# Kernel optimization log

Hardware: AMD Instinct MI355X
Metric: run time of the kernel (lower is better)

The kernel has to match this reference:

```python
import jax, jax.numpy as jnp
import numpy as np

D_MODEL = 1024
NHEAD = 16
D_FF = 4096
SEQ = 2048
BATCH = 2
EPS = 1e-5


def _layernorm(x, g, b):
    mu = jnp.mean(x, axis=-1, keepdims=True)
    var = jnp.var(x, axis=-1, keepdims=True)
    return (x - mu) * jax.lax.rsqrt(var + EPS) * g + b


def setup_inputs() -> dict:
    key = jax.random.key(0)
    ks = jax.random.split(key, 16)
    s = 0.02
    def lin(k, din, dout):
        return jax.random.normal(k, (din, dout), jnp.float32) * s
    return {
        "x": jax.random.normal(ks[0], (SEQ, BATCH, D_MODEL), jnp.float32),
        "Wq": lin(ks[1], D_MODEL, D_MODEL), "bq": jnp.zeros((D_MODEL,), jnp.float32),
        "Wk": lin(ks[2], D_MODEL, D_MODEL), "bk": jnp.zeros((D_MODEL,), jnp.float32),
        "Wv": lin(ks[3], D_MODEL, D_MODEL), "bv": jnp.zeros((D_MODEL,), jnp.float32),
        "Wo": lin(ks[4], D_MODEL, D_MODEL), "bo": jnp.zeros((D_MODEL,), jnp.float32),
        "W1": lin(ks[5], D_MODEL, D_FF), "b1": jnp.zeros((D_FF,), jnp.float32),
        "W2": lin(ks[6], D_FF, D_MODEL), "b2": jnp.zeros((D_MODEL,), jnp.float32),
        "g1": jnp.ones((D_MODEL,), jnp.float32), "be1": jnp.zeros((D_MODEL,), jnp.float32),
        "g2": jnp.ones((D_MODEL,), jnp.float32), "be2": jnp.zeros((D_MODEL,), jnp.float32),
    }


def reference(x, Wq, bq, Wk, bk, Wv, bv, Wo, bo, W1, b1, W2, b2, g1, be1, g2, be2):
    # batch_first=False: x is [S, B, D] -> [B, S, D]
    xb = jnp.transpose(x, (1, 0, 2))
    B, S, D = xb.shape
    H, Dh = NHEAD, D // NHEAD

    Q = (xb @ Wq + bq).reshape(B, S, H, Dh)
    K = (xb @ Wk + bk).reshape(B, S, H, Dh)
    V = (xb @ Wv + bv).reshape(B, S, H, Dh)

    scores = jnp.einsum('bqhd,bkhd->bhqk', Q, K) / jnp.sqrt(jnp.float32(Dh))
    attn = jax.nn.softmax(scores, axis=-1)
    ctx = jnp.einsum('bhqk,bkhd->bqhd', attn, V).reshape(B, S, D)

    x_att = ctx @ Wo + bo
    xb = xb + x_att
    xb = _layernorm(xb, g1, be1)  # post-norm (norm_first=False)

    h = jax.nn.gelu(xb @ W1 + b1, approximate=False)
    xb = xb + (h @ W2 + b2)
    xb = _layernorm(xb, g2, be2)

    return jnp.transpose(xb, (1, 0, 2))  # back to [S, B, D]
```

## Files before the change

### kernel.cpp

```cpp
#include <hip/hip_runtime.h>
#include <hip/hip_bf16.h>
#include <cstdint>
#include <cstddef>

#define S_LEN 2048
#define BATCHN 2
#define DMODEL 1024
#define NHEADS 16
#define DHEAD 64
#define DFF 4096
#define NTOK (S_LEN*BATCHN)

typedef __bf16 bf16x8 __attribute__((ext_vector_type(8)));
typedef __bf16 bf16x4 __attribute__((ext_vector_type(4)));
typedef float f32x4 __attribute__((ext_vector_type(4)));
typedef __hip_bfloat16 bf16s;

#define QSCALE 0.18033688011112042592f

__device__ static inline void gload_lds16(const void* g, void* l) {
  __builtin_amdgcn_global_load_lds((const __attribute__((address_space(1))) void*)g,
                                   (__attribute__((address_space(3))) void*)l,
                                   16, 0, 0);
}


__global__ __launch_bounds__(256) void transpose_convert4(const float* __restrict__ s0,
                                                          const float* __restrict__ s1,
                                                          const float* __restrict__ s2,
                                                          const float* __restrict__ s3,
                                                          bf16s* __restrict__ dst) {
  __shared__ float tile[32][33];
  const float* in = (blockIdx.z == 0) ? s0 : (blockIdx.z == 1) ? s1 : (blockIdx.z == 2) ? s2 : s3;
  bf16s* out = dst + (size_t)blockIdx.z * DMODEL * DMODEL;
  const int tx = threadIdx.x & 31;
  const int ty = threadIdx.x >> 5;
  const int bx = blockIdx.x * 32;
  const int by = blockIdx.y * 32;
#pragma unroll
  for (int i = 0; i < 32; i += 8)
    tile[ty + i][tx] = in[(size_t)(by + ty + i) * DMODEL + bx + tx];
  __syncthreads();
#pragma unroll
  for (int i = 0; i < 32; i += 8)
    out[(size_t)(bx + ty + i) * DMODEL + by + tx] = __float2bfloat16(tile[tx][ty + i]);
}

__global__ __launch_bounds__(256) void transpose_convert(const float* __restrict__ in,
                                                         bf16s* __restrict__ out,
                                                         int K, int N) {
  __shared__ float tile[32][33];
  const int tx = threadIdx.x & 31;
  const int ty = threadIdx.x >> 5;
  const int bx = blockIdx.x * 32;
  const int by = blockIdx.y * 32;
#pragma unroll
  for (int i = 0; i < 32; i += 8)
    tile[ty + i][tx] = in[(size_t)(by + ty + i) * N + bx + tx];
  __syncthreads();
#pragma unroll
  for (int i = 0; i < 32; i += 8)
    out[(size_t)(bx + ty + i) * K + by + tx] = __float2bfloat16(tile[tx][ty + i]);
}

__global__ __launch_bounds__(256) void cvt_bf16_kernel(const float* __restrict__ in,
                                                       bf16s* __restrict__ out, int n4) {
  int i = blockIdx.x * 256 + threadIdx.x;
  if (i < n4) {
    float4 v = ((const float4*)in)[i];
    union { bf16s h[4]; uint2 u; } pk;
    pk.h[0] = __float2bfloat16(v.x); pk.h[1] = __float2bfloat16(v.y);
    pk.h[2] = __float2bfloat16(v.z); pk.h[3] = __float2bfloat16(v.w);
    ((uint2*)out)[i] = pk.u;
  }
}

__global__ __launch_bounds__(256) void bias_concat_kernel(const float* __restrict__ bq,
                                                          const float* __restrict__ bk,
                                                          const float* __restrict__ bv,
                                                          float* __restrict__ bqkv) {
  int i = blockIdx.x * 256 + threadIdx.x;
  if (i < 3 * DMODEL) {
    float v = (i < DMODEL) ? bq[i] : (i < 2 * DMODEL ? bk[i - DMODEL] : bv[i - 2 * DMODEL]);
    bqkv[i] = v;
  }
}

template<int EPI>
__global__ __launch_bounds__(256, 3)
void gemm_kernel(const bf16s* __restrict__ A, const bf16s* __restrict__ Bt,
                 int N, int K, int kchunk,
                 const float* __restrict__ bias,
                 float* __restrict__ outF, bf16s* __restrict__ outB,
                 bf16s* __restrict__ Qb, bf16s* __restrict__ Kb, bf16s* __restrict__ Vtb)
{
  __shared__ bf16s smem[2][8192];
  const int tid = threadIdx.x;
  const int l = tid & 63, w = tid >> 6;
  const int m0 = blockIdx.y * 128;
  const int n0 = blockIdx.x * 128;
  const int kbeg = blockIdx.z * kchunk;
  const int lr = l & 15, lg = l >> 4;
  const int wm = (w >> 1) * 64, wn = (w & 1) * 64;

  const int off0 = (w * 2 + 0) * 1024 + l * 16;
  const int off1 = (w * 2 + 1) * 1024 + l * 16;
  const char* a0 = (const char*)(A + (size_t)(m0 + (off0 >> 6)) * K + kbeg) + (off0 & 63);
  const char* a1 = (const char*)(A + (size_t)(m0 + (off1 >> 6)) * K + kbeg) + (off1 & 63);
  const char* b0 = (const char*)(Bt + (size_t)(n0 + (off0 >> 6)) * K + kbeg) + (off0 & 63);
  const char* b1 = (const char*)(Bt + (size_t)(n0 + (off1 >> 6)) * K + kbeg) + (off1 & 63);

  f32x4 acc[4][4] = {};

  auto stage = [&](int buf, int t) {
    char* s = (char*)&smem[buf][0];
    size_t kb = (size_t)t * 64;
    gload_lds16(a0 + kb, s + off0);
    gload_lds16(a1 + kb, s + off1);
    gload_lds16(b0 + kb, s + 8192 + off0);
    gload_lds16(b1 + kb, s + 8192 + off1);
  };

  const int ao = (wm + lr) * 64 + lg * 16;
  const int bo = 8192 + (wn + lr) * 64 + lg * 16;

  auto compute = [&](int buf) {
    const char* base = (const char*)&smem[buf][0];
    bf16x8 af[4], bfr[4];
#pragma unroll
    for (int mi = 0; mi < 4; ++mi) af[mi] = *(const bf16x8*)(base + ao + mi * 1024);
#pragma unroll
    for (int ni = 0; ni < 4; ++ni) bfr[ni] = *(const bf16x8*)(base + bo + ni * 1024);
#pragma unroll
    for (int mi = 0; mi < 4; ++mi)
#pragma unroll
      for (int ni = 0; ni < 4; ++ni)
        acc[mi][ni] = __builtin_amdgcn_mfma_f32_16x16x32_bf16(af[mi], bfr[ni], acc[mi][ni], 0, 0, 0);
  };

  const int nt = kchunk / 32;
  stage(0, 0);
  __syncthreads();
  int cur = 0;
  for (int t = 0; t < nt - 1; ++t) {
    stage(cur ^ 1, t + 1);
    compute(cur);
    __syncthreads();
    cur ^= 1;
  }
  compute(cur);

  float* outFz = (EPI == 1) ? outF + (size_t)blockIdx.z * ((size_t)NTOK * DMODEL) : outF;
#pragma unroll
  for (int mi = 0; mi < 4; ++mi) {
#pragma unroll
    for (int ni = 0; ni < 4; ++ni) {
#pragma unroll
      for (int r = 0; r < 4; ++r) {
        int row = m0 + wm + mi * 16 + lg * 4 + r;
        int col = n0 + wn + ni * 16 + lr;
        float v = acc[mi][ni][r];
        if (EPI == 0) {
          v += bias[col];
          int which = col >> 10;
          int h = (col & 1023) >> 6;
          int d = col & 63;
          int b = row & 1;
          int s = row >> 1;
          if (which == 0)
            Qb[(((size_t)(b * NHEADS + h)) * S_LEN + s) * DHEAD + d] = __float2bfloat16(v * QSCALE);
          else if (which == 1)
            Kb[(((size_t)(b * NHEADS + h)) * S_LEN + s) * DHEAD + d] = __float2bfloat16(v);
          else
            Vtb[(((size_t)(b * NHEADS + h)) * DHEAD + d) * S_LEN + s] = __float2bfloat16(v);
        } else if (EPI == 1) {
          outFz[(size_t)row * N + col] = v;
        } else {
          v += bias[col];
          float gv = 0.5f * v * (1.0f + erff(v * 0.70710678118654752f));
          outB[(size_t)row * N + col] = __float2bfloat16(gv);
        }
      }
    }
  }
}

__global__ __launch_bounds__(256, 2)
void attn_kernel(const bf16s* __restrict__ Qb, const bf16s* __restrict__ Kb,
                 const bf16s* __restrict__ Vtb, bf16s* __restrict__ ctx)
{
  __shared__ __align__(1024) char lds[51200];
  const int tid = threadIdx.x;
  const int l = tid & 63, w = tid >> 6;
  const int lr = l & 15, lg = l >> 4;

  int lin = blockIdx.x;
  int wg = (lin & 7) * 64 + (lin >> 3);
  int qb = wg & 15;
  int hb = wg >> 4;
  int h = hb & 15, b = hb >> 4;

  const char* Qg = (const char*)(Qb + ((size_t)(b * NHEADS + h)) * S_LEN * DHEAD);
  const char* Kg = (const char*)(Kb + ((size_t)(b * NHEADS + h)) * S_LEN * DHEAD);
  const char* Vg = (const char*)(Vtb + ((size_t)(b * NHEADS + h)) * DHEAD * S_LEN);

  const int swz = (lr & 7) << 4;
  const int aK0 = lr * 128 + ((lg * 16) ^ swz);
  const int aK1 = lr * 128 + ((64 + lg * 16) ^ swz);
  const int klane = (l >> 3) * 128  + (((l & 7) * 16) ^ ((l & 56) << 1));
  const int vlane = (l >> 3) * 4096 + (((l & 7) * 16) ^ ((l & 56) << 1));
  const int l16 = l * 16;
  char* Pw = lds + 32768 + w * 4608;
  const int pwA = lr * 144 + lg * 8;
  const int prA = lr * 144 + lg * 16;

  const int q0 = qb * 128 + w * 32;
  bf16x8 aq[2][2];
#pragma unroll
  for (int qi = 0; qi < 2; ++qi)
#pragma unroll
    for (int kk = 0; kk < 2; ++kk)
      aq[qi][kk] = *(const bf16x8*)(Qg + (size_t)(q0 + qi * 16 + lr) * 128 + kk * 64 + lg * 16);

  f32x4 o0[4] = {}, o1[4] = {};
  float m0 = -1e30f, m1 = -1e30f;
  float ls0 = 0.f, ls1 = 0.f;

  const int NT = S_LEN / 64;

  auto stage = [&](char* dK, int tile) {
    const char* kbg = Kg + (size_t)tile * 8192;
    const char* vbg = Vg + (size_t)tile * 128;
    char* dV = dK + 8192;
#pragma unroll
    for (int i = 0; i < 2; ++i) {
      int c = w * 2 + i;
      gload_lds16(kbg + c * 1024 + klane, dK + c * 1024 + l16);
      gload_lds16(vbg + (size_t)c * 32768 + vlane, dV + c * 1024 + l16);
    }
  };

  stage(lds, 0);
  asm volatile("s_waitcnt vmcnt(0)" ::: "memory");
  __builtin_amdgcn_s_barrier();

#define ATTN_ITER(BUF, t)                                                        \
  {                                                                              \
    int nxt = ((t) + 1 < NT) ? (t) + 1 : NT - 1;                                 \
    stage(lds + ((BUF) ^ 1) * 16384, nxt);                                       \
    const char* bK = lds + (BUF) * 16384;                                        \
    const char* bV = bK + 8192;                                                  \
    f32x4 st0[4], st1[4];                                                        \
    _Pragma("unroll")                                                            \
    for (int ni = 0; ni < 4; ++ni) {                                             \
      bf16x8 k0 = *(const bf16x8*)(bK + ni * 2048 + aK0);                        \
      bf16x8 k1 = *(const bf16x8*)(bK + ni * 2048 + aK1);                        \
      f32x4 z = {};                                                              \
      st0[ni] = __builtin_amdgcn_mfma_f32_16x16x32_bf16(k0, aq[0][0], z, 0, 0, 0);\
      st0[ni] = __builtin_amdgcn_mfma_f32_16x16x32_bf16(k1, aq[0][1], st0[ni], 0, 0, 0);\
      st1[ni] = __builtin_amdgcn_mfma_f32_16x16x32_bf16(k0, aq[1][0], z, 0, 0, 0);\
      st1[ni] = __builtin_amdgcn_mfma_f32_16x16x32_bf16(k1, aq[1][1], st1[ni], 0, 0, 0);\
    }                                                                            \
    f32x4 vm0 = st0[0], vm1 = st1[0];                                            \
    _Pragma("unroll")                                                            \
    for (int ni = 1; ni < 4; ++ni) {                                             \
      _Pragma("unroll")                                                          \
      for (int r = 0; r < 4; ++r) {                                              \
        vm0[r] = fmaxf(vm0[r], st0[ni][r]);                                      \
        vm1[r] = fmaxf(vm1[r], st1[ni][r]);                                      \
      }                                                                          \
    }                                                                            \
    float mx0 = fmaxf(fmaxf(vm0[0], vm0[1]), fmaxf(vm0[2], vm0[3]));             \
    float mx1 = fmaxf(fmaxf(vm1[0], vm1[1]), fmaxf(vm1[2], vm1[3]));             \
    mx0 = fmaxf(mx0, __shfl_xor(mx0, 16)); mx0 = fmaxf(mx0, __shfl_xor(mx0, 32));\
    mx1 = fmaxf(mx1, __shfl_xor(mx1, 16)); mx1 = fmaxf(mx1, __shfl_xor(mx1, 32));\
    if (!__all(mx0 <= m0 + 8.f && mx1 <= m1 + 8.f)) {                            \
      float nm0 = fmaxf(m0, mx0), nm1 = fmaxf(m1, mx1);                          \
      float al0 = exp2f(m0 - nm0), al1 = exp2f(m1 - nm1);                        \
      m0 = nm0; m1 = nm1; ls0 *= al0; ls1 *= al1;                                \
      _Pragma("unroll")                                                          \
      for (int r = 0; r < 4; ++r) {                                              \
        float s0r = __shfl(al0, lg * 4 + r);                                     \
        float s1r = __shfl(al1, lg * 4 + r);                                     \
        _Pragma("unroll")                                                        \
        for (int di = 0; di < 4; ++di) { o0[di][r] *= s0r; o1[di][r] *= s1r; }   \
      }                                                                          \
    }                                                                            \
    f32x4 ac0 = {}, ac1 = {};                                                    \
    _Pragma("unroll")                                                            \
    for (int ni = 0; ni < 4; ++ni) {                                             \
      _Pragma("unroll")                                                          \
      for (int r = 0; r < 4; ++r) {                                              \
        st0[ni][r] = exp2f(st0[ni][r] - m0);                                     \
        st1[ni][r] = exp2f(st1[ni][r] - m1);                                     \
      }                                                                          \
      ac0 += st0[ni]; ac1 += st1[ni];                                            \
    }                                                                            \
    ls0 += ac0[0] + ac0[1] + ac0[2] + ac0[3];                                    \
    ls1 += ac1[0] + ac1[1] + ac1[2] + ac1[3];                                    \
    _Pragma("unroll")                                                            \
    for (int ni = 0; ni < 4; ++ni) {                                             \
      bf16x4 p0, p1;                                                             \
      _Pragma("unroll")                                                          \
      for (int j = 0; j < 4; ++j) { p0[j] = (__bf16)st0[ni][j]; p1[j] = (__bf16)st1[ni][j]; }\
      *(bf16x4*)(Pw + pwA + ni * 32) = p0;                                       \
      *(bf16x4*)(Pw + 2304 + pwA + ni * 32) = p1;                                \
    }                                                                            \
    _Pragma("unroll")                                                            \
    for (int kk = 0; kk < 2; ++kk) {                                             \
      bf16x8 ap0 = *(const bf16x8*)(Pw + prA + kk * 64);                         \
      bf16x8 ap1 = *(const bf16x8*)(Pw + 2304 + prA + kk * 64);                  \
      const int av = kk ? aK1 : aK0;                                             \
      _Pragma("unroll")                                                          \
      for (int di = 0; di < 4; ++di) {                                           \
        bf16x8 vv = *(const bf16x8*)(bV + di * 2048 + av);                       \
        o0[di] = __builtin_amdgcn_mfma_f32_16x16x32_bf16(ap0, vv, o0[di], 0, 0, 0);\
        o1[di] = __builtin_amdgcn_mfma_f32_16x16x32_bf16(ap1, vv, o1[di], 0, 0, 0);\
      }                                                                          \
    }                                                                            \
    asm volatile("s_waitcnt vmcnt(0)" ::: "memory");                             \
    __builtin_amdgcn_s_barrier();                                                \
  }

  for (int t = 0; t < NT; t += 2) {
    ATTN_ITER(0, t);
    ATTN_ITER(1, t + 1);
  }
#undef ATTN_ITER

#pragma unroll
  for (int qi = 0; qi < 2; ++qi) {
    float ls = qi ? ls1 : ls0;
    ls += __shfl_xor(ls, 16);
    ls += __shfl_xor(ls, 32);
    float inv = 1.0f / ls;
#pragma unroll
    for (int r = 0; r < 4; ++r) {
      float invr = __shfl(inv, lg * 4 + r);
      int srow = q0 + qi * 16 + lg * 4 + r;
      int tkn = srow * BATCHN + b;
#pragma unroll
      for (int di = 0; di < 4; ++di) {
        int d = h * DHEAD + di * 16 + lr;
        float v = (qi ? o1[di][r] : o0[di][r]) * invr;
        ctx[(size_t)tkn * DMODEL + d] = __float2bfloat16(v);
      }
    }
  }
}

template<int WB>
__global__ __launch_bounds__(256)
void ln_kernel(const float* __restrict__ inA, const float* __restrict__ inB,
               const float* __restrict__ resid, const float* __restrict__ bias,
               const float* __restrict__ g, const float* __restrict__ be,
               float* __restrict__ outF, bf16s* __restrict__ outB)
{
  const int row = blockIdx.x;
  const int tid = threadIdx.x;
  const size_t base = (size_t)row * DMODEL;
  float4 a = ((const float4*)(inA + base))[tid];
  float4 bq = ((const float4*)(inB + base))[tid];
  float4 rr = ((const float4*)(resid + base))[tid];
  float4 bi = ((const float4*)bias)[tid];
  float4 v;
  v.x = a.x + bq.x + rr.x + bi.x;
  v.y = a.y + bq.y + rr.y + bi.y;
  v.z = a.z + bq.z + rr.z + bi.z;
  v.w = a.w + bq.w + rr.w + bi.w;
  float s = v.x + v.y + v.z + v.w;
  float s2 = v.x * v.x + v.y * v.y + v.z * v.z + v.w * v.w;
#pragma unroll
  for (int m = 1; m < 64; m <<= 1) { s += __shfl_xor(s, m); s2 += __shfl_xor(s2, m); }
  __shared__ float sm[8];
  const int wv = tid >> 6, l = tid & 63;
  if (l == 0) { sm[wv] = s; sm[4 + wv] = s2; }
  __syncthreads();
  s = sm[0] + sm[1] + sm[2] + sm[3];
  s2 = sm[4] + sm[5] + sm[6] + sm[7];
  float mean = s * (1.0f / DMODEL);
  float var = s2 * (1.0f / DMODEL) - mean * mean;
  float rstd = rsqrtf(var + 1e-5f);
  float4 gv = ((const float4*)g)[tid];
  float4 bv = ((const float4*)be)[tid];
  float o0 = (v.x - mean) * rstd * gv.x + bv.x;
  float o1 = (v.y - mean) * rstd * gv.y + bv.y;
  float o2 = (v.z - mean) * rstd * gv.z + bv.z;
  float o3 = (v.w - mean) * rstd * gv.w + bv.w;
  float4 ov = {o0, o1, o2, o3};
  ((float4*)(outF + base))[tid] = ov;
  if (WB) {
    union { bf16s h[4]; uint2 u; } pk;
    pk.h[0] = __float2bfloat16(o0); pk.h[1] = __float2bfloat16(o1);
    pk.h[2] = __float2bfloat16(o2); pk.h[3] = __float2bfloat16(o3);
    ((uint2*)(outB + base))[tid] = pk.u;
  }
}

extern "C" void kernel_launch(void* const* d_in, const int* in_sizes, int n_in,
                              void* d_out, int out_size, void* d_ws, size_t ws_size,
                              hipStream_t stream) {
  const float* x  = (const float*)d_in[0];
  const float* Wq = (const float*)d_in[1];
  const float* bq = (const float*)d_in[2];
  const float* Wk = (const float*)d_in[3];
  const float* bk = (const float*)d_in[4];
  const float* Wv = (const float*)d_in[5];
  const float* bv = (const float*)d_in[6];
  const float* Wo = (const float*)d_in[7];
  const float* bo = (const float*)d_in[8];
  const float* W1 = (const float*)d_in[9];
  const float* b1 = (const float*)d_in[10];
  const float* W2 = (const float*)d_in[11];
  const float* b2 = (const float*)d_in[12];
  const float* g1 = (const float*)d_in[13];
  const float* be1 = (const float*)d_in[14];
  const float* g2 = (const float*)d_in[15];
  const float* be2 = (const float*)d_in[16];

  char* ws = (char*)d_ws;
  size_t off = 0;
  auto alloc = [&](size_t bytes) -> void* {
    void* p = ws + off;
    off += (bytes + 255) & ~(size_t)255;
    return p;
  };
  bf16s* Wqkv_t = (bf16s*)alloc((size_t)3 * DMODEL * DMODEL * 2);
  bf16s* Wo_t   = (bf16s*)alloc((size_t)DMODEL * DMODEL * 2);
  bf16s* W1_t   = (bf16s*)alloc((size_t)DFF * DMODEL * 2);
  bf16s* W2_t   = (bf16s*)alloc((size_t)DMODEL * DFF * 2);
  float* bqkv   = (float*)alloc((size_t)3 * DMODEL * 4);
  bf16s* Xb     = (bf16s*)alloc((size_t)NTOK * DMODEL * 2);
  bf16s* Qb     = (bf16s*)alloc((size_t)NTOK * DMODEL * 2);
  bf16s* Kb     = (bf16s*)alloc((size_t)NTOK * DMODEL * 2);
  bf16s* Vtb    = (bf16s*)alloc((size_t)NTOK * DMODEL * 2);
  bf16s* ctx    = (bf16s*)alloc((size_t)NTOK * DMODEL * 2);
  float* sAB    = (float*)alloc((size_t)2 * NTOK * DMODEL * 4);
  bf16s* y1     = (bf16s*)alloc((size_t)NTOK * DMODEL * 2);
  float* y1f    = (float*)alloc((size_t)NTOK * DMODEL * 4);
  bf16s* Hb     = Qb;
  if (off > ws_size) return;

  float* sA = sAB;
  float* sB = sAB + (size_t)NTOK * DMODEL;

  transpose_convert4<<<dim3(32, 32, 4), 256, 0, stream>>>(Wq, Wk, Wv, Wo, Wqkv_t);
  transpose_convert<<<dim3(DFF / 32, DMODEL / 32), 256, 0, stream>>>(W1, W1_t, DMODEL, DFF);
  transpose_convert<<<dim3(DMODEL / 32, DFF / 32), 256, 0, stream>>>(W2, W2_t, DFF, DMODEL);
  bias_concat_kernel<<<12, 256, 0, stream>>>(bq, bk, bv, bqkv);
  cvt_bf16_kernel<<<(NTOK * DMODEL / 4 + 255) / 256, 256, 0, stream>>>(x, Xb, NTOK * DMODEL / 4);

  gemm_kernel<0><<<dim3(24, 32, 1), 256, 0, stream>>>(
      Xb, Wqkv_t, 3 * DMODEL, DMODEL, DMODEL, bqkv, nullptr, nullptr, Qb, Kb, Vtb);

  attn_kernel<<<512, 256, 0, stream>>>(Qb, Kb, Vtb, ctx);

  gemm_kernel<1><<<dim3(8, 32, 2), 256, 0, stream>>>(
      ctx, Wo_t, DMODEL, DMODEL, DMODEL / 2, nullptr, sAB, nullptr, nullptr, nullptr, nullptr);
  ln_kernel<1><<<NTOK, 256, 0, stream>>>(sA, sB, x, bo, g1, be1, y1f, y1);
  gemm_kernel<2><<<dim3(32, 32, 1), 256, 0, stream>>>(
      y1, W1_t, DFF, DMODEL, DMODEL, b1, nullptr, Hb, nullptr, nullptr, nullptr);
  gemm_kernel<1><<<dim3(8, 32, 2), 256, 0, stream>>>(
      Hb, W2_t, DMODEL, DFF, DFF / 2, nullptr, sAB, nullptr, nullptr, nullptr, nullptr);
  ln_kernel<0><<<NTOK, 256, 0, stream>>>(sA, sB, y1f, b2, g2, be2, (float*)d_out, nullptr);
}
```

Measured before the change: 390.5 us.

## Replace GEMM with 256x256-tile, 8-wave, 4-stage pipelined swizzled kernel

```diff
diff --git a/kernel.cpp b/kernel.cpp
--- a/kernel.cpp
+++ b/kernel.cpp
@@ -10,6 +10,7 @@
 #define DHEAD 64
 #define DFF 4096
 #define NTOK (S_LEN*BATCHN)
+#define MB (1u<<20)
 
 typedef __bf16 bf16x8 __attribute__((ext_vector_type(8)));
 typedef __bf16 bf16x4 __attribute__((ext_vector_type(4)));
@@ -87,78 +88,105 @@
 }
 
 template<int EPI>
-__global__ __launch_bounds__(256, 3)
-void gemm_kernel(const bf16s* __restrict__ A, const bf16s* __restrict__ Bt,
-                 int N, int K, int kchunk,
-                 const float* __restrict__ bias,
-                 float* __restrict__ outF, bf16s* __restrict__ outB,
-                 bf16s* __restrict__ Qb, bf16s* __restrict__ Kb, bf16s* __restrict__ Vtb)
+__global__ __launch_bounds__(512, 2)
+void gemm8p_kernel(const bf16s* __restrict__ A, const bf16s* __restrict__ Bt,
+                   int N, int K, int kchunk, int gx, int plane,
+                   const float* __restrict__ bias,
+                   float* __restrict__ outF, bf16s* __restrict__ outB,
+                   bf16s* __restrict__ Qb, bf16s* __restrict__ Kb, bf16s* __restrict__ Vtb)
 {
-  __shared__ bf16s smem[2][8192];
+  __shared__ __align__(1024) char lds[131072];
   const int tid = threadIdx.x;
   const int l = tid & 63, w = tid >> 6;
-  const int m0 = blockIdx.y * 128;
-  const int n0 = blockIdx.x * 128;
-  const int kbeg = blockIdx.z * kchunk;
   const int lr = l & 15, lg = l >> 4;
-  const int wm = (w >> 1) * 64, wn = (w & 1) * 64;
-
-  const int off0 = (w * 2 + 0) * 1024 + l * 16;
-  const int off1 = (w * 2 + 1) * 1024 + l * 16;
-  const char* a0 = (const char*)(A + (size_t)(m0 + (off0 >> 6)) * K + kbeg) + (off0 & 63);
-  const char* a1 = (const char*)(A + (size_t)(m0 + (off1 >> 6)) * K + kbeg) + (off1 & 63);
-  const char* b0 = (const char*)(Bt + (size_t)(n0 + (off0 >> 6)) * K + kbeg) + (off0 & 63);
-  const char* b1 = (const char*)(Bt + (size_t)(n0 + (off1 >> 6)) * K + kbeg) + (off1 & 63);
-
-  f32x4 acc[4][4] = {};
-
-  auto stage = [&](int buf, int t) {
-    char* s = (char*)&smem[buf][0];
-    size_t kb = (size_t)t * 64;
-    gload_lds16(a0 + kb, s + off0);
-    gload_lds16(a1 + kb, s + off1);
-    gload_lds16(b0 + kb, s + 8192 + off0);
-    gload_lds16(b1 + kb, s + 8192 + off1);
+  const int wr = w >> 2, wc = w & 3;
+
+  const int nb = gridDim.x;
+  const int lin = blockIdx.x;
+  const int sw = (lin & 7) * (nb >> 3) + (lin >> 3);
+  const int bz = sw / plane;
+  const int tpl = sw - bz * plane;
+  const int by = tpl / gx, bx = tpl - by * gx;
+  const int m0 = by * 256, n0 = bx * 256, kbeg = bz * kchunk;
+  const int NKH = kchunk >> 5;
+
+  const char* Ab = (const char*)A + ((size_t)m0 * K + kbeg) * 2;
+  const char* Bb = (const char*)Bt + ((size_t)n0 * K + kbeg) * 2;
+  const size_t Krow = (size_t)K * 2;
+
+  f32x4 acc[8][4] = {};
+
+  auto stageH = [&](int h) {
+    if (h >= 2 * NKH) return;
+    const int n = h >> 1;
+    char* dst = lds + (n & 3) * 32768 + (h & 1) * 16384;
+    const char* src = (h & 1) ? Bb : Ab;
+#pragma unroll
+    for (int c = 0; c < 2; ++c) {
+      int L = c * 8192 + tid * 16;
+      int U = L ^ (((L >> 6) & 3) << 4);
+      gload_lds16(src + (size_t)(U >> 6) * Krow + (size_t)n * 64 + (U & 63), dst + L);
+    }
   };
 
-  const int ao = (wm + lr) * 64 + lg * 16;
-  const int bo = 8192 + (wn + lr) * 64 + lg * 16;
-
-  auto compute = [&](int buf) {
-    const char* base = (const char*)&smem[buf][0];
-    bf16x8 af[4], bfr[4];
-#pragma unroll
-    for (int mi = 0; mi < 4; ++mi) af[mi] = *(const bf16x8*)(base + ao + mi * 1024);
-#pragma unroll
-    for (int ni = 0; ni < 4; ++ni) bfr[ni] = *(const bf16x8*)(base + bo + ni * 1024);
+  const int swzc = (lr & 3) << 4;
+  const int kcol = (lg * 16) ^ swzc;
+  const int aoff = (wr * 128 + lr) * 64;
+  const int boff = 16384 + (wc * 64 + lr) * 64;
+
+#pragma unroll
+  for (int h = 0; h < 6; ++h) stageH(h);
+  asm volatile("s_waitcnt vmcnt(8)" ::: "memory");
+  __builtin_amdgcn_s_barrier();
+
+  for (int n = 0; n < NKH; ++n) {
+    const char* slab = lds + (n & 3) * 32768;
+    stageH(2 * n + 6);
+    bf16x8 bf[4], af[4];
+#pragma unroll
+    for (int ni = 0; ni < 4; ++ni) bf[ni] = *(const bf16x8*)(slab + boff + ni * 1024 + kcol);
+#pragma unroll
+    for (int mi = 0; mi < 4; ++mi) af[mi] = *(const bf16x8*)(slab + aoff + mi * 1024 + kcol);
+    __builtin_amdgcn_s_barrier();
+    asm volatile("s_waitcnt lgkmcnt(0)" ::: "memory");
+    __builtin_amdgcn_sched_barrier(0);
+    __builtin_amdgcn_s_setprio(1);
 #pragma unroll
     for (int mi = 0; mi < 4; ++mi)
 #pragma unroll
       for (int ni = 0; ni < 4; ++ni)
-        acc[mi][ni] = __builtin_amdgcn_mfma_f32_16x16x32_bf16(af[mi], bfr[ni], acc[mi][ni], 0, 0, 0);
-  };
-
-  const int nt = kchunk / 32;
-  stage(0, 0);
-  __syncthreads();
-  int cur = 0;
-  for (int t = 0; t < nt - 1; ++t) {
-    stage(cur ^ 1, t + 1);
-    compute(cur);
-    __syncthreads();
-    cur ^= 1;
-  }
-  compute(cur);
-
-  float* outFz = (EPI == 1) ? outF + (size_t)blockIdx.z * ((size_t)NTOK * DMODEL) : outF;
-#pragma unroll
-  for (int mi = 0; mi < 4; ++mi) {
+        acc[mi][ni] = __builtin_amdgcn_mfma_f32_16x16x32_bf16(af[mi], bf[ni], acc[mi][ni], 0, 0, 0);
+    __builtin_amdgcn_s_setprio(0);
+    __builtin_amdgcn_s_barrier();
+    stageH(2 * n + 7);
+#pragma unroll
+    for (int mi = 0; mi < 4; ++mi) af[mi] = *(const bf16x8*)(slab + aoff + 4096 + mi * 1024 + kcol);
+    if (n + 1 < NKH) {
+      if (n + 1 == NKH - 1) asm volatile("s_waitcnt vmcnt(0)" ::: "memory");
+      else                  asm volatile("s_waitcnt vmcnt(4)" ::: "memory");
+    }
+    __builtin_amdgcn_s_barrier();
+    asm volatile("s_waitcnt lgkmcnt(0)" ::: "memory");
+    __builtin_amdgcn_sched_barrier(0);
+    __builtin_amdgcn_s_setprio(1);
+#pragma unroll
+    for (int mi = 0; mi < 4; ++mi)
+#pragma unroll
+      for (int ni = 0; ni < 4; ++ni)
+        acc[4 + mi][ni] = __builtin_amdgcn_mfma_f32_16x16x32_bf16(af[mi], bf[ni], acc[4 + mi][ni], 0, 0, 0);
+    __builtin_amdgcn_s_setprio(0);
+    __builtin_amdgcn_s_barrier();
+  }
+
+  float* outFz = outF + (size_t)bz * ((size_t)NTOK * DMODEL);
+#pragma unroll
+  for (int mi = 0; mi < 8; ++mi) {
 #pragma unroll
     for (int ni = 0; ni < 4; ++ni) {
 #pragma unroll
       for (int r = 0; r < 4; ++r) {
-        int row = m0 + wm + mi * 16 + lg * 4 + r;
-        int col = n0 + wn + ni * 16 + lr;
+        int row = m0 + wr * 128 + mi * 16 + lg * 4 + r;
+        int col = n0 + wc * 64 + ni * 16 + lr;
         float v = acc[mi][ni][r];
         if (EPI == 0) {
           v += bias[col];
@@ -419,30 +447,23 @@
   const float* be2 = (const float*)d_in[16];
 
   char* ws = (char*)d_ws;
-  size_t off = 0;
-  auto alloc = [&](size_t bytes) -> void* {
-    void* p = ws + off;
-    off += (bytes + 255) & ~(size_t)255;
-    return p;
-  };
-  bf16s* Wqkv_t = (bf16s*)alloc((size_t)3 * DMODEL * DMODEL * 2);
-  bf16s* Wo_t   = (bf16s*)alloc((size_t)DMODEL * DMODEL * 2);
-  bf16s* W1_t   = (bf16s*)alloc((size_t)DFF * DMODEL * 2);
-  bf16s* W2_t   = (bf16s*)alloc((size_t)DMODEL * DFF * 2);
-  float* bqkv   = (float*)alloc((size_t)3 * DMODEL * 4);
-  bf16s* Xb     = (bf16s*)alloc((size_t)NTOK * DMODEL * 2);
-  bf16s* Qb     = (bf16s*)alloc((size_t)NTOK * DMODEL * 2);
-  bf16s* Kb     = (bf16s*)alloc((size_t)NTOK * DMODEL * 2);
-  bf16s* Vtb    = (bf16s*)alloc((size_t)NTOK * DMODEL * 2);
-  bf16s* ctx    = (bf16s*)alloc((size_t)NTOK * DMODEL * 2);
-  float* sAB    = (float*)alloc((size_t)2 * NTOK * DMODEL * 4);
-  bf16s* y1     = (bf16s*)alloc((size_t)NTOK * DMODEL * 2);
-  float* y1f    = (float*)alloc((size_t)NTOK * DMODEL * 4);
-  bf16s* Hb     = Qb;
-  if (off > ws_size) return;
-
-  float* sA = sAB;
-  float* sB = sAB + (size_t)NTOK * DMODEL;
+  if (ws_size < (size_t)113 * MB) return;
+  bf16s* Wqkv_t = (bf16s*)(ws + (size_t)0 * MB);
+  bf16s* Wo_t   = (bf16s*)(ws + (size_t)6 * MB);
+  bf16s* W1_t   = (bf16s*)(ws + (size_t)8 * MB);
+  bf16s* W2_t   = (bf16s*)(ws + (size_t)16 * MB);
+  float* bqkv   = (float*)(ws + (size_t)24 * MB);
+  bf16s* Xb     = (bf16s*)(ws + (size_t)25 * MB);
+  bf16s* y1     = (bf16s*)(ws + (size_t)25 * MB);
+  bf16s* Qb     = (bf16s*)(ws + (size_t)33 * MB);
+  bf16s* Kb     = (bf16s*)(ws + (size_t)41 * MB);
+  bf16s* Vtb    = (bf16s*)(ws + (size_t)49 * MB);
+  bf16s* ctx    = (bf16s*)(ws + (size_t)57 * MB);
+  bf16s* Hb     = (bf16s*)(ws + (size_t)33 * MB);
+  float* p01    = (float*)(ws + (size_t)65 * MB);
+  float* y1f    = (float*)(ws + (size_t)97 * MB);
+  float* p0 = p01;
+  float* p1 = p01 + (size_t)NTOK * DMODEL;
 
   transpose_convert4<<<dim3(32, 32, 4), 256, 0, stream>>>(Wq, Wk, Wv, Wo, Wqkv_t);
   transpose_convert<<<dim3(DFF / 32, DMODEL / 32), 256, 0, stream>>>(W1, W1_t, DMODEL, DFF);
@@ -450,17 +471,21 @@
   bias_concat_kernel<<<12, 256, 0, stream>>>(bq, bk, bv, bqkv);
   cvt_bf16_kernel<<<(NTOK * DMODEL / 4 + 255) / 256, 256, 0, stream>>>(x, Xb, NTOK * DMODEL / 4);
 
-  gemm_kernel<0><<<dim3(24, 32, 1), 256, 0, stream>>>(
-      Xb, Wqkv_t, 3 * DMODEL, DMODEL, DMODEL, bqkv, nullptr, nullptr, Qb, Kb, Vtb);
+  gemm8p_kernel<0><<<192, 512, 0, stream>>>(
+      Xb, Wqkv_t, 3 * DMODEL, DMODEL, DMODEL, 12, 192, bqkv,
+      nullptr, nullptr, Qb, Kb, Vtb);
 
   attn_kernel<<<512, 256, 0, stream>>>(Qb, Kb, Vtb, ctx);
 
-  gemm_kernel<1><<<dim3(8, 32, 2), 256, 0, stream>>>(
-      ctx, Wo_t, DMODEL, DMODEL, DMODEL / 2, nullptr, sAB, nullptr, nullptr, nullptr, nullptr);
-  ln_kernel<1><<<NTOK, 256, 0, stream>>>(sA, sB, x, bo, g1, be1, y1f, y1);
-  gemm_kernel<2><<<dim3(32, 32, 1), 256, 0, stream>>>(
-      y1, W1_t, DFF, DMODEL, DMODEL, b1, nullptr, Hb, nullptr, nullptr, nullptr);
-  gemm_kernel<1><<<dim3(8, 32, 2), 256, 0, stream>>>(
-      Hb, W2_t, DMODEL, DFF, DFF / 2, nullptr, sAB, nullptr, nullptr, nullptr, nullptr);
-  ln_kernel<0><<<NTOK, 256, 0, stream>>>(sA, sB, y1f, b2, g2, be2, (float*)d_out, nullptr);
-}
+  gemm8p_kernel<1><<<128, 512, 0, stream>>>(
+      ctx, Wo_t, DMODEL, DMODEL, DMODEL / 2, 4, 64, nullptr,
+      p01, nullptr, nullptr, nullptr, nullptr);
+  ln_kernel<1><<<NTOK, 256, 0, stream>>>(p0, p1, x, bo, g1, be1, y1f, y1);
+  gemm8p_kernel<2><<<256, 512, 0, stream>>>(
+      y1, W1_t, DFF, DMODEL, DMODEL, 16, 256, b1,
+      nullptr, Hb, nullptr, nullptr, nullptr);
+  gemm8p_kernel<1><<<128, 512, 0, stream>>>(
+      Hb, W2_t, DMODEL, DFF, DFF / 2, 4, 64, nullptr,
+      p01, nullptr, nullptr, nullptr, nullptr);
+  ln_kernel<0><<<NTOK, 256, 0, stream>>>(p0, p1, y1f, b2, g2, be2, (float*)d_out, nullptr);
+}
```

Result: slower. 443.6 us (+13.6%).
